# Kernel optimization log

Measured on AMD Instinct MI355X. Metric: run time of the kernel, lower is better.

Reference implementation:

```python
import jax, jax.numpy as jnp
import numpy as np


def setup_inputs() -> dict:
    key = jax.random.key(0)
    ks = jax.random.split(key, 7)
    B, C, N, F = 4, 8, 2048, 64
    H, O = 64, 64
    s_in = 1.0 / np.sqrt(F)
    s_h = 1.0 / np.sqrt(H)
    return {
        "x": jax.random.normal(ks[0], (B, C, N, F), dtype=jnp.float32),
        "W1": jax.random.uniform(ks[1], (H, F), jnp.float32, -s_in, s_in),
        "b1": jax.random.uniform(ks[2], (H,), jnp.float32, -s_in, s_in),
        "W2": jax.random.uniform(ks[3], (H, F), jnp.float32, -s_in, s_in),
        "b2": jax.random.uniform(ks[4], (H,), jnp.float32, -s_in, s_in),
        "W3": jax.random.uniform(ks[5], (O, F), jnp.float32, -s_in, s_in),
        "b3": jax.random.uniform(ks[6], (O,), jnp.float32, -s_in, s_in),
    }


def reference(x, W1, b1, W2, b2, W3, b3):
    # e1, e2: [B,C,N,H]  (torch Linear: x @ W^T + b)
    e1 = jnp.einsum("bcnf,hf->bcnh", x, W1) + b1
    e2 = jnp.einsum("bcnf,hf->bcnh", x, W2) + b2
    # adjacency via ReLU(e1 @ e2^T): [B,C,N,N]
    adj = jax.nn.relu(jnp.einsum("bcnh,bcmh->bcnm", e1, e2))
    # propagate: [B,C,N,F]
    h = jnp.einsum("bcnm,bcmf->bcnf", adj, x)
    # output projection (linear3): [B,C,N,O]
    return jnp.einsum("bcnf,of->bcno", h, W3) + b3
```

## Files before the change

kernel.cpp:

```cpp
#include <hip/hip_runtime.h>
#include <hip/hip_bf16.h>

#define BCH 32
#define NN  2048
#define DD  64

typedef __attribute__((ext_vector_type(8)))  __bf16 bf16x8;
typedef __attribute__((ext_vector_type(4)))  __bf16 bf16x4;
typedef __attribute__((ext_vector_type(4)))  float  f32x4;
typedef __attribute__((ext_vector_type(16))) float  f32x16;
typedef __attribute__((ext_vector_type(2)))  int    i32x2;
typedef __attribute__((ext_vector_type(4)))  int    i32x4;
typedef __attribute__((ext_vector_type(2)))  unsigned int u32x2;

__device__ inline f32x4 mfma16(bf16x8 a, bf16x8 b, f32x4 c) {
    return __builtin_amdgcn_mfma_f32_16x16x32_bf16(a, b, c, 0, 0, 0);
}
__device__ inline f32x16 mfma32(bf16x8 a, bf16x8 b, f32x16 c) {
    return __builtin_amdgcn_mfma_f32_32x32x16_bf16(a, b, c, 0, 0, 0);
}
__device__ inline void plswap(int& a, int& b) {
    u32x2 r = __builtin_amdgcn_permlane32_swap((unsigned)a, (unsigned)b, false, false);
    a = (int)r[0];
    b = (int)r[1];
}

__global__ __launch_bounds__(256) void prep_kernel(
    const float* __restrict__ x,
    const float* __restrict__ W1, const float* __restrict__ b1,
    const float* __restrict__ W2, const float* __restrict__ b2,
    const float* __restrict__ W3,
    __bf16* __restrict__ e1f, __bf16* __restrict__ e2f, __bf16* __restrict__ vtf)
{
    const int t   = threadIdx.x;
    const int blk = blockIdx.x;
    const int bc  = blk >> 5, st = blk & 31;
    const long grow = (long)bc * NN + st * 64;
    const int w = t >> 6, l = t & 63, lg = l >> 4, li = l & 15;

    bf16x8 a[4][2];
    #pragma unroll
    for (int nb = 0; nb < 4; ++nb)
        #pragma unroll
        for (int kk = 0; kk < 2; ++kk) {
            const float* p = x + (grow + nb * 16 + li) * DD + kk * 32 + lg * 8;
            f32x4 v0 = *(const f32x4*)p, v1 = *(const f32x4*)(p + 4);
            #pragma unroll
            for (int j = 0; j < 4; ++j) {
                a[nb][kk][j]     = (__bf16)v0[j];
                a[nb][kk][4 + j] = (__bf16)v1[j];
            }
        }

    bf16x8 wf1[2], wf2[2], wf3[2];
    #pragma unroll
    for (int kk = 0; kk < 2; ++kk) {
        const float* p1 = W1 + (w * 16 + li) * DD + kk * 32 + lg * 8;
        const float* p2 = W2 + (w * 16 + li) * DD + kk * 32 + lg * 8;
        const float* p3 = W3 + (w * 16 + li) * DD + kk * 32 + lg * 8;
        f32x4 u0 = *(const f32x4*)p1, u1 = *(const f32x4*)(p1 + 4);
        f32x4 v0 = *(const f32x4*)p2, v1 = *(const f32x4*)(p2 + 4);
        f32x4 t0 = *(const f32x4*)p3, t1 = *(const f32x4*)(p3 + 4);
        #pragma unroll
        for (int j = 0; j < 4; ++j) {
            wf1[kk][j] = (__bf16)u0[j]; wf1[kk][4 + j] = (__bf16)u1[j];
            wf2[kk][j] = (__bf16)v0[j]; wf2[kk][4 + j] = (__bf16)v1[j];
            wf3[kk][j] = (__bf16)t0[j]; wf3[kk][4 + j] = (__bf16)t1[j];
        }
    }
    const f32x4 bq1 = *(const f32x4*)(b1 + w * 16 + lg * 4);
    const f32x4 bq2 = *(const f32x4*)(b2 + w * 16 + lg * 4);

    const size_t tbase = (size_t)(bc * 32 + st) * 4096;

    #pragma unroll
    for (int nb = 0; nb < 4; ++nb) {
        f32x4 acc1 = {0.f,0.f,0.f,0.f}, acc2 = {0.f,0.f,0.f,0.f}, acc3 = {0.f,0.f,0.f,0.f};
        #pragma unroll
        for (int kk = 0; kk < 2; ++kk) {
            acc1 = mfma16(wf1[kk], a[nb][kk], acc1);
            acc2 = mfma16(wf2[kk], a[nb][kk], acc2);
            acc3 = mfma16(a[nb][kk], wf3[kk], acc3);
        }
        bf16x4 q1, q2, q3;
        #pragma unroll
        for (int r = 0; r < 4; ++r) {
            q1[r] = (__bf16)(acc1[r] + bq1[r]);
            q2[r] = (__bf16)(acc2[r] + bq2[r]);
            q3[r] = (__bf16)acc3[r];
        }
        *(bf16x4*)&e1f[tbase + (w * 2 + (lg >> 1)) * 512 + (nb * 16 + li) * 8 + (lg & 1) * 4] = q1;
        *(bf16x4*)&e2f[tbase + (w * 2 + (lg >> 1)) * 512 + (nb * 16 + li) * 8 + (lg & 1) * 4] = q2;
        *(bf16x4*)&vtf[tbase + (nb * 2 + (lg >> 1)) * 512 + (w * 16 + li) * 8 + (lg & 1) * 4] = q3;
    }
}

__global__ __launch_bounds__(128, 2) void fused_kernel(
    const __bf16* __restrict__ e1f, const __bf16* __restrict__ e2f,
    const __bf16* __restrict__ vtf, const float* __restrict__ b3,
    float* __restrict__ out)
{
    __shared__ float scratch[4096];

    const int t   = threadIdx.x;
    const int bid = blockIdx.x;
    const int x8 = bid & 7, jj = bid >> 3;
    const int bc = x8 * 4 + (jj & 3), nt = jj >> 2;

    const int wm = t >> 6, l = t & 63;
    const int l31 = l & 31, hi5 = l >> 5;
    const int nbase = nt * 64;

    const float bv0 = b3[l31], bv1 = b3[32 + l31];

    bf16x8 e1v[2][4];
    #pragma unroll
    for (int nb = 0; nb < 2; ++nb) {
        const __bf16* p = e1f + ((size_t)bc * 32 + nt) * 4096 + hi5 * 512 + (nb * 32 + l31) * 8;
        #pragma unroll
        for (int kk = 0; kk < 4; ++kk)
            e1v[nb][kk] = *(const bf16x8*)(p + kk * 1024);
    }

    f32x16 fz;
    #pragma unroll
    for (int i = 0; i < 16; ++i) fz[i] = 0.f;
    f32x16 hacc[2][2];
    #pragma unroll
    for (int nb = 0; nb < 2; ++nb)
        #pragma unroll
        for (int fb = 0; fb < 2; ++fb)
            #pragma unroll
            for (int i = 0; i < 16; ++i) hacc[nb][fb][i] = 0.f;

    const __bf16* E2 = e2f + (size_t)bc * 131072 + hi5 * 512 + (wm * 32 + l31) * 8;
    const __bf16* VT = vtf + (size_t)bc * 131072 + (wm * 4 + hi5) * 512 + l31 * 8;

    auto loadEF = [&](int kt, bf16x8 (&ef)[4]) {
        const __bf16* p = E2 + (size_t)kt * 4096;
        #pragma unroll
        for (int kk = 0; kk < 4; ++kk)
            ef[kk] = *(const bf16x8*)(p + kk * 1024);
    };
    auto loadVF = [&](int kt, bf16x8 (&vf)[4]) {
        const __bf16* p = VT + (size_t)kt * 4096;
        #pragma unroll
        for (int kk2 = 0; kk2 < 2; ++kk2) {
            vf[kk2 * 2 + 0] = *(const bf16x8*)(p + kk2 * 1024);
            vf[kk2 * 2 + 1] = *(const bf16x8*)(p + kk2 * 1024 + 256);
        }
    };
    auto computeS = [&](bf16x8 (&ef)[4], f32x16 (&sT)[2]) {
        sT[0] = mfma32(ef[0], e1v[0][0], fz);
        sT[1] = mfma32(ef[0], e1v[1][0], fz);
        #pragma unroll
        for (int kk = 1; kk < 4; ++kk) {
            sT[0] = mfma32(ef[kk], e1v[0][kk], sT[0]);
            sT[1] = mfma32(ef[kk], e1v[1][kk], sT[1]);
        }
    };
    auto packQ = [&](const f32x16 (&sT)[2], i32x2 (&Q)[2][4]) {
        #pragma unroll
        for (int nb = 0; nb < 2; ++nb)
            #pragma unroll
            for (int g = 0; g < 4; ++g) {
                bf16x4 q0;
                #pragma unroll
                for (int r = 0; r < 4; ++r)
                    q0[r] = (__bf16)fmaxf(sT[nb][4 * g + r], 0.f);
                Q[nb][g] = __builtin_bit_cast(i32x2, q0);
            }
    };
    auto doPV = [&](i32x2 (&Q)[2][4], bf16x8 (&vf)[4]) {
        #pragma unroll
        for (int kk2 = 0; kk2 < 2; ++kk2)
            #pragma unroll
            for (int nb = 0; nb < 2; ++nb) {
                int a0 = Q[nb][2 * kk2][0],     a1 = Q[nb][2 * kk2][1];
                int b0 = Q[nb][2 * kk2 + 1][0], b1 = Q[nb][2 * kk2 + 1][1];
                plswap(a0, b0);
                plswap(a1, b1);
                i32x4 pfi = { a0, a1, b0, b1 };
                bf16x8 pf = __builtin_bit_cast(bf16x8, pfi);
                hacc[nb][0] = mfma32(pf, vf[kk2 * 2 + 0], hacc[nb][0]);
                hacc[nb][1] = mfma32(pf, vf[kk2 * 2 + 1], hacc[nb][1]);
            }
    };

    bf16x8 efA[4], vfA[4], efB[4], vfB[4];
    i32x2 Qa[2][4], Qb[2][4];
    f32x16 sT[2];

    loadEF(0, efA); loadVF(0, vfA);
    for (int kt = 0; kt < 32; kt += 2) {
        loadEF(kt + 1, efB); loadVF(kt + 1, vfB);
        computeS(efA, sT);
        packQ(sT, Qa);
        doPV(Qa, vfA);
        if (kt + 2 < 32) { loadEF(kt + 2, efA); loadVF(kt + 2, vfA); }
        computeS(efB, sT);
        packQ(sT, Qb);
        doPV(Qb, vfB);
    }

    if (wm == 1) {
        #pragma unroll
        for (int nb = 0; nb < 2; ++nb)
            #pragma unroll
            for (int q = 0; q < 8; ++q) {
                f32x4 v;
                #pragma unroll
                for (int r = 0; r < 4; ++r) {
                    const int idx = q * 4 + r;
                    v[r] = hacc[nb][idx >> 4][idx & 15];
                }
                *(f32x4*)&scratch[nb * 2048 + q * 256 + l * 4] = v;
            }
    }
    __syncthreads();
    if (wm == 0) {
        #pragma unroll
        for (int nb = 0; nb < 2; ++nb)
            #pragma unroll
            for (int q = 0; q < 8; ++q) {
                f32x4 v = *(const f32x4*)&scratch[nb * 2048 + q * 256 + l * 4];
                #pragma unroll
                for (int r = 0; r < 4; ++r) {
                    const int idx = q * 4 + r;
                    hacc[nb][idx >> 4][idx & 15] += v[r];
                }
            }
        #pragma unroll
        for (int nb = 0; nb < 2; ++nb) {
            const size_t ob = ((size_t)bc * NN + nbase + nb * 32) * DD;
            #pragma unroll
            for (int reg = 0; reg < 16; ++reg) {
                const int n = (reg & 3) + 8 * (reg >> 2) + 4 * hi5;
                out[ob + (size_t)n * DD + l31]      = hacc[nb][0][reg] + bv0;
                out[ob + (size_t)n * DD + 32 + l31] = hacc[nb][1][reg] + bv1;
            }
        }
    }
}

extern "C" void kernel_launch(void* const* d_in, const int* in_sizes, int n_in,
                              void* d_out, int out_size, void* d_ws, size_t ws_size,
                              hipStream_t stream) {
    const float* x  = (const float*)d_in[0];
    const float* W1 = (const float*)d_in[1];
    const float* b1 = (const float*)d_in[2];
    const float* W2 = (const float*)d_in[3];
    const float* b2 = (const float*)d_in[4];
    const float* W3 = (const float*)d_in[5];
    const float* b3 = (const float*)d_in[6];
    float* out = (float*)d_out;

    __bf16* e1f = (__bf16*)d_ws;
    __bf16* e2f = e1f + (size_t)BCH * NN * DD;
    __bf16* vtf = e2f + (size_t)BCH * NN * DD;

    prep_kernel<<<dim3(1024), dim3(256), 0, stream>>>(x, W1, b1, W2, b2, W3, e1f, e2f, vtf);
    fused_kernel<<<dim3(1024), dim3(128), 0, stream>>>(e1f, e2f, vtf, b3, out);
}
```

Measured before the change: 59.33 us.

## Share E2/V tiles across four row-waves via LDS with async global_load_lds double buffering

The fused kernel moves from 128-thread blocks covering one 64-row tile to 512-thread blocks covering four 64-row tiles of the same batch-channel. Each E2 and V key tile is staged once into LDS with global_load_lds and double buffered, so all eight waves share it instead of each wave loading it from global memory into registers. MFMA sections are wrapped in s_setprio, and the final cross-wave reduction is done in two rounds through the reused LDS. The aim is less global/L2 traffic, at the cost of per-iteration block barriers, a grid of only 256 blocks, and LDS read latency on the critical path.

```diff
diff --git a/kernel.cpp b/kernel.cpp
--- a/kernel.cpp
+++ b/kernel.cpp
@@ -18,6 +18,11 @@
 }
 __device__ inline f32x16 mfma32(bf16x8 a, bf16x8 b, f32x16 c) {
     return __builtin_amdgcn_mfma_f32_32x32x16_bf16(a, b, c, 0, 0, 0);
+}
+__device__ inline void gload16(const void* g, void* l) {
+    __builtin_amdgcn_global_load_lds(
+        (const __attribute__((address_space(1))) void*)g,
+        (__attribute__((address_space(3))) void*)l, 16, 0, 0);
 }
 __device__ inline void plswap(int& a, int& b) {
     u32x2 r = __builtin_amdgcn_permlane32_swap((unsigned)a, (unsigned)b, false, false);
@@ -95,28 +100,30 @@
     }
 }
 
-__global__ __launch_bounds__(128, 2) void fused_kernel(
+__global__ __launch_bounds__(512, 1) void fused_kernel(
     const __bf16* __restrict__ e1f, const __bf16* __restrict__ e2f,
     const __bf16* __restrict__ vtf, const float* __restrict__ b3,
     float* __restrict__ out)
 {
-    __shared__ float scratch[4096];
+    __shared__ __align__(16) __bf16 tile[2][8192];
 
     const int t   = threadIdx.x;
     const int bid = blockIdx.x;
-    const int x8 = bid & 7, jj = bid >> 3;
-    const int bc = x8 * 4 + (jj & 3), nt = jj >> 2;
-
-    const int wm = t >> 6, l = t & 63;
+    const int j5  = bid & 31;
+    const int bc  = (j5 & 7) * 4 + (j5 >> 3);
+    const int nt  = bid >> 5;
+
+    const int w = t >> 6, l = t & 63;
+    const int wn = w & 3, wm = w >> 2;
     const int l31 = l & 31, hi5 = l >> 5;
-    const int nbase = nt * 64;
+    const int nbase = nt * 256 + wn * 64;
 
     const float bv0 = b3[l31], bv1 = b3[32 + l31];
 
     bf16x8 e1v[2][4];
     #pragma unroll
     for (int nb = 0; nb < 2; ++nb) {
-        const __bf16* p = e1f + ((size_t)bc * 32 + nt) * 4096 + hi5 * 512 + (nb * 32 + l31) * 8;
+        const __bf16* p = e1f + ((size_t)bc * 32 + nt * 4 + wn) * 4096 + hi5 * 512 + (nb * 32 + l31) * 8;
         #pragma unroll
         for (int kk = 0; kk < 4; ++kk)
             e1v[nb][kk] = *(const bf16x8*)(p + kk * 1024);
@@ -133,24 +140,34 @@
             #pragma unroll
             for (int i = 0; i < 16; ++i) hacc[nb][fb][i] = 0.f;
 
-    const __bf16* E2 = e2f + (size_t)bc * 131072 + hi5 * 512 + (wm * 32 + l31) * 8;
-    const __bf16* VT = vtf + (size_t)bc * 131072 + (wm * 4 + hi5) * 512 + l31 * 8;
-
-    auto loadEF = [&](int kt, bf16x8 (&ef)[4]) {
-        const __bf16* p = E2 + (size_t)kt * 4096;
+    const __bf16* E2T = e2f + (size_t)bc * 131072;
+    const __bf16* VTT = vtf + (size_t)bc * 131072;
+
+    auto stage = [&](int buf, int kt) {
+        gload16(E2T + (size_t)kt * 4096 + t * 8, &tile[buf][w * 512]);
+        gload16(VTT + (size_t)kt * 4096 + t * 8, &tile[buf][4096 + w * 512]);
+    };
+
+    stage(0, 0);
+
+    for (int kt = 0; kt < 32; ++kt) {
+        const int buf = kt & 1;
+        if (kt + 1 < 32) {
+            stage(buf ^ 1, kt + 1);
+            asm volatile("s_waitcnt vmcnt(2)" ::: "memory");
+        } else {
+            asm volatile("s_waitcnt vmcnt(0)" ::: "memory");
+        }
+        __builtin_amdgcn_sched_barrier(0);
+        __builtin_amdgcn_s_barrier();
+
+        bf16x8 ef[4];
         #pragma unroll
         for (int kk = 0; kk < 4; ++kk)
-            ef[kk] = *(const bf16x8*)(p + kk * 1024);
-    };
-    auto loadVF = [&](int kt, bf16x8 (&vf)[4]) {
-        const __bf16* p = VT + (size_t)kt * 4096;
-        #pragma unroll
-        for (int kk2 = 0; kk2 < 2; ++kk2) {
-            vf[kk2 * 2 + 0] = *(const bf16x8*)(p + kk2 * 1024);
-            vf[kk2 * 2 + 1] = *(const bf16x8*)(p + kk2 * 1024 + 256);
-        }
-    };
-    auto computeS = [&](bf16x8 (&ef)[4], f32x16 (&sT)[2]) {
+            ef[kk] = *(const bf16x8*)&tile[buf][kk * 1024 + hi5 * 512 + (wm * 32 + l31) * 8];
+
+        f32x16 sT[2];
+        __builtin_amdgcn_s_setprio(1);
         sT[0] = mfma32(ef[0], e1v[0][0], fz);
         sT[1] = mfma32(ef[0], e1v[1][0], fz);
         #pragma unroll
@@ -158,8 +175,9 @@
             sT[0] = mfma32(ef[kk], e1v[0][kk], sT[0]);
             sT[1] = mfma32(ef[kk], e1v[1][kk], sT[1]);
         }
-    };
-    auto packQ = [&](const f32x16 (&sT)[2], i32x2 (&Q)[2][4]) {
+        __builtin_amdgcn_s_setprio(0);
+
+        i32x2 Q[2][4];
         #pragma unroll
         for (int nb = 0; nb < 2; ++nb)
             #pragma unroll
@@ -170,8 +188,14 @@
                     q0[r] = (__bf16)fmaxf(sT[nb][4 * g + r], 0.f);
                 Q[nb][g] = __builtin_bit_cast(i32x2, q0);
             }
-    };
-    auto doPV = [&](i32x2 (&Q)[2][4], bf16x8 (&vf)[4]) {
+
+        bf16x8 vf[4];
+        #pragma unroll
+        for (int kk2 = 0; kk2 < 2; ++kk2) {
+            vf[kk2 * 2 + 0] = *(const bf16x8*)&tile[buf][4096 + (wm * 4 + hi5) * 512 + kk2 * 1024 + l31 * 8];
+            vf[kk2 * 2 + 1] = *(const bf16x8*)&tile[buf][4096 + (wm * 4 + hi5) * 512 + kk2 * 1024 + 256 + l31 * 8];
+        }
+        __builtin_amdgcn_s_setprio(1);
         #pragma unroll
         for (int kk2 = 0; kk2 < 2; ++kk2)
             #pragma unroll
@@ -185,59 +209,51 @@
                 hacc[nb][0] = mfma32(pf, vf[kk2 * 2 + 0], hacc[nb][0]);
                 hacc[nb][1] = mfma32(pf, vf[kk2 * 2 + 1], hacc[nb][1]);
             }
-    };
-
-    bf16x8 efA[4], vfA[4], efB[4], vfB[4];
-    i32x2 Qa[2][4], Qb[2][4];
-    f32x16 sT[2];
-
-    loadEF(0, efA); loadVF(0, vfA);
-    for (int kt = 0; kt < 32; kt += 2) {
-        loadEF(kt + 1, efB); loadVF(kt + 1, vfB);
-        computeS(efA, sT);
-        packQ(sT, Qa);
-        doPV(Qa, vfA);
-        if (kt + 2 < 32) { loadEF(kt + 2, efA); loadVF(kt + 2, vfA); }
-        computeS(efB, sT);
-        packQ(sT, Qb);
-        doPV(Qb, vfB);
-    }
-
-    if (wm == 1) {
-        #pragma unroll
-        for (int nb = 0; nb < 2; ++nb)
-            #pragma unroll
-            for (int q = 0; q < 8; ++q) {
-                f32x4 v;
-                #pragma unroll
-                for (int r = 0; r < 4; ++r) {
-                    const int idx = q * 4 + r;
-                    v[r] = hacc[nb][idx >> 4][idx & 15];
+        __builtin_amdgcn_s_setprio(0);
+
+        __builtin_amdgcn_s_barrier();
+    }
+
+    float* scratch = (float*)&tile[0][0];
+    #pragma unroll
+    for (int r2 = 0; r2 < 2; ++r2) {
+        __syncthreads();
+        if ((wn >> 1) == r2 && wm == 1) {
+            #pragma unroll
+            for (int nb = 0; nb < 2; ++nb)
+                #pragma unroll
+                for (int q = 0; q < 8; ++q) {
+                    f32x4 v;
+                    #pragma unroll
+                    for (int r = 0; r < 4; ++r) {
+                        const int idx = q * 4 + r;
+                        v[r] = hacc[nb][idx >> 4][idx & 15];
+                    }
+                    *(f32x4*)&scratch[(wn & 1) * 4096 + nb * 2048 + q * 256 + l * 4] = v;
                 }
-                *(f32x4*)&scratch[nb * 2048 + q * 256 + l * 4] = v;
-            }
-    }
-    __syncthreads();
-    if (wm == 0) {
-        #pragma unroll
-        for (int nb = 0; nb < 2; ++nb)
-            #pragma unroll
-            for (int q = 0; q < 8; ++q) {
-                f32x4 v = *(const f32x4*)&scratch[nb * 2048 + q * 256 + l * 4];
-                #pragma unroll
-                for (int r = 0; r < 4; ++r) {
-                    const int idx = q * 4 + r;
-                    hacc[nb][idx >> 4][idx & 15] += v[r];
+        }
+        __syncthreads();
+        if ((wn >> 1) == r2 && wm == 0) {
+            #pragma unroll
+            for (int nb = 0; nb < 2; ++nb)
+                #pragma unroll
+                for (int q = 0; q < 8; ++q) {
+                    f32x4 v = *(const f32x4*)&scratch[(wn & 1) * 4096 + nb * 2048 + q * 256 + l * 4];
+                    #pragma unroll
+                    for (int r = 0; r < 4; ++r) {
+                        const int idx = q * 4 + r;
+                        hacc[nb][idx >> 4][idx & 15] += v[r];
+                    }
                 }
-            }
-        #pragma unroll
-        for (int nb = 0; nb < 2; ++nb) {
-            const size_t ob = ((size_t)bc * NN + nbase + nb * 32) * DD;
-            #pragma unroll
-            for (int reg = 0; reg < 16; ++reg) {
-                const int n = (reg & 3) + 8 * (reg >> 2) + 4 * hi5;
-                out[ob + (size_t)n * DD + l31]      = hacc[nb][0][reg] + bv0;
-                out[ob + (size_t)n * DD + 32 + l31] = hacc[nb][1][reg] + bv1;
+            #pragma unroll
+            for (int nb = 0; nb < 2; ++nb) {
+                const size_t ob = ((size_t)bc * NN + nbase + nb * 32) * DD;
+                #pragma unroll
+                for (int reg = 0; reg < 16; ++reg) {
+                    const int n = (reg & 3) + 8 * (reg >> 2) + 4 * hi5;
+                    out[ob + (size_t)n * DD + l31]      = hacc[nb][0][reg] + bv0;
+                    out[ob + (size_t)n * DD + 32 + l31] = hacc[nb][1][reg] + bv1;
+                }
             }
         }
     }
@@ -260,5 +276,5 @@
     __bf16* vtf = e2f + (size_t)BCH * NN * DD;
 
     prep_kernel<<<dim3(1024), dim3(256), 0, stream>>>(x, W1, b1, W2, b2, W3, e1f, e2f, vtf);
-    fused_kernel<<<dim3(1024), dim3(128), 0, stream>>>(e1f, e2f, vtf, b3, out);
-}
+    fused_kernel<<<dim3(256), dim3(512), 0, stream>>>(e1f, e2f, vtf, b3, out);
+}
```

New measurement: 59.56 us. Within noise of the previous version (+0.4%).
